# Performance work log

Measured on AMD Instinct MI355X. Metric: run time of the kernel, lower is better.

Reference implementation:

```python
import jax, jax.numpy as jnp
import numpy as np

N, T = 512, 48
VOCAB, EMBED, HIDDEN, IMG_DIM = 32000, 1024, 1024, 4096


def setup_inputs() -> dict:
    key = jax.random.key(0)
    ks = jax.random.split(key, 12)
    s = 0.02
    return {
        "questions": jax.random.randint(ks[0], (N, T), 0, VOCAB, dtype=jnp.int32),
        "img_features": jax.random.normal(ks[1], (N, IMG_DIM), dtype=jnp.float32),
        "emb": jax.random.normal(ks[2], (VOCAB, EMBED), dtype=jnp.float32) * s,
        "W_img": jax.random.normal(ks[3], (HIDDEN, IMG_DIM), dtype=jnp.float32) * s,
        "b_img": jnp.zeros((HIDDEN,), dtype=jnp.float32),
        "W_ih": jax.random.normal(ks[4], (4 * HIDDEN, EMBED), dtype=jnp.float32) * s,
        "W_hh": jax.random.normal(ks[5], (4 * HIDDEN, HIDDEN), dtype=jnp.float32) * s,
        "b_ih": jnp.zeros((4 * HIDDEN,), dtype=jnp.float32),
        "b_hh": jnp.zeros((4 * HIDDEN,), dtype=jnp.float32),
        "W_out": jax.random.normal(ks[6], (VOCAB, HIDDEN), dtype=jnp.float32) * s,
        "b_out": jnp.zeros((VOCAB,), dtype=jnp.float32),
        "first_words": 1,
    }


def reference(questions, img_features, emb, W_img, b_img, W_ih, W_hh, b_ih, b_hh,
              W_out, b_out, first_words):
    H = W_hh.shape[1]
    n = questions.shape[0]
    emb_q = emb[questions].transpose(1, 0, 2)          # [T, N, E]
    emb_i = img_features @ W_img.T + b_img             # [N, H]
    if first_words:
        seq = jnp.concatenate([emb_i[None], emb_q], axis=0)   # [T+1, N, E]
    else:
        seq = jnp.concatenate([emb_q, emb_i[None]], axis=0)

    def cell(carry, x_t):
        h, c = carry
        gates = x_t @ W_ih.T + b_ih + h @ W_hh.T + b_hh   # [N, 4H]
        i, f, g, o = jnp.split(gates, 4, axis=-1)          # torch LSTMCell gate order
        i, f, o = jax.nn.sigmoid(i), jax.nn.sigmoid(f), jax.nn.sigmoid(o)
        g = jnp.tanh(g)
        c = f * c + i * g
        h = o * jnp.tanh(c)
        return (h, c), h

    h0 = jnp.zeros((n, H), dtype=seq.dtype)
    (_, _), hs = jax.lax.scan(cell, (h0, h0), seq)     # hs: [T+1, N, H]
    hidden_states = hs.transpose(1, 0, 2)              # [N, T+1, H]
    output = hidden_states[:, -1, :] @ W_out.T + b_out  # [N, vocab]
    return output, hidden_states
```

## Files before the change

### kernel.cpp

```cpp
#include <hip/hip_runtime.h>
#include <hip/hip_bf16.h>
#include <stdint.h>

typedef __bf16 bf16_t;
typedef __attribute__((ext_vector_type(8))) __bf16 bf16x8;
typedef __attribute__((ext_vector_type(4))) __bf16 bf16x4;
typedef __attribute__((ext_vector_type(4))) float f32x4;
#define LL long long

__device__ __forceinline__ void gl_lds16(const bf16_t* g, bf16_t* s) {
  __builtin_amdgcn_global_load_lds(
      (const __attribute__((address_space(1))) void*)g,
      (__attribute__((address_space(3))) void*)s, 16, 0, 0);
}

__device__ __forceinline__ float sigm(float x) {
  return 1.0f / (1.0f + __expf(-x));
}
__device__ __forceinline__ float tanh_s(float x) {
  float e = __expf(-2.0f * fabsf(x));
  float t = (1.0f - e) / (1.0f + e);
  return copysignf(t, x);
}

template<int BM, int OUTBF>
__global__ __launch_bounds__(256, 2)
void gemm_bt(const bf16_t* __restrict__ A, const bf16_t* __restrict__ B,
             const float* __restrict__ bias,
             bf16_t* __restrict__ Cb, float* __restrict__ Cf,
             int N, int K, const int* __restrict__ fw, LL off0, LL off1) {
  __shared__ bf16_t lds_a[BM * 32];
  __shared__ bf16_t lds_b[128 * 32];
  const int tid = threadIdx.x;
  const int w = tid >> 6, l = tid & 63;
  const LL m0 = (LL)blockIdx.x * BM;
  const LL n0 = (LL)blockIdx.y * 128;
  constexpr int MI = BM / 32;
  const int wm = w & 1, wn = w >> 1;
  f32x4 acc[MI][4] = {};

  const int srow = l >> 2;
  const int scol = (l & 3) * 8;

  for (int kt = 0; kt < K; kt += 32) {
    for (int c = w; c < BM / 16; c += 4)
      gl_lds16(A + (m0 + c * 16 + srow) * K + kt + scol, &lds_a[c * 512]);
#pragma unroll
    for (int j = 0; j < 2; ++j) {
      int c = w * 2 + j;
      gl_lds16(B + (n0 + c * 16 + srow) * K + kt + scol, &lds_b[c * 512]);
    }
    __syncthreads();
    const int fr = l & 15, fk = (l >> 4) * 8;
    bf16x8 af[MI], bfr[4];
#pragma unroll
    for (int i = 0; i < MI; ++i)
      af[i] = *(const bf16x8*)&lds_a[(wm * (BM / 2) + i * 16 + fr) * 32 + fk];
#pragma unroll
    for (int j = 0; j < 4; ++j)
      bfr[j] = *(const bf16x8*)&lds_b[(wn * 64 + j * 16 + fr) * 32 + fk];
#pragma unroll
    for (int i = 0; i < MI; ++i)
#pragma unroll
      for (int j = 0; j < 4; ++j)
        acc[i][j] = __builtin_amdgcn_mfma_f32_16x16x32_bf16(af[i], bfr[j],
                                                            acc[i][j], 0, 0, 0);
    __syncthreads();
  }

  const LL coff = (fw[0] ? off1 : off0);
  const int er = (l >> 4) * 4, ec = l & 15;
#pragma unroll
  for (int i = 0; i < MI; ++i) {
#pragma unroll
    for (int j = 0; j < 4; ++j) {
      LL mrow = m0 + wm * (BM / 2) + i * 16 + er;
      LL ncol = n0 + wn * 64 + j * 16 + ec;
      float bs = bias[ncol];
#pragma unroll
      for (int r = 0; r < 4; ++r) {
        float v = acc[i][j][r] + bs;
        if (OUTBF) Cb[coff + (mrow + r) * N + ncol] = (bf16_t)v;
        else       Cf[(mrow + r) * N + ncol] = v;
      }
    }
  }
}

__global__ __launch_bounds__(256, 2)
void lstm_step(const bf16_t* __restrict__ h_in, const bf16_t* __restrict__ Whh,
               const bf16_t* __restrict__ Gt, float* __restrict__ c,
               bf16_t* __restrict__ h_out, float* __restrict__ hid, int t) {
  __shared__ bf16_t lds_a[64 * 32];
  __shared__ bf16_t lds_b[128 * 32];
  __shared__ float lds_ex[64 * 128];
  const int tid = threadIdx.x;
  const int w = tid >> 6, l = tid & 63;
  const int m0 = blockIdx.x * 64;
  const int n0 = blockIdx.y * 128;
  const int wm = w & 1, wn = w >> 1;
  f32x4 acc[2][4] = {};
  const int srow = l >> 2, scol = (l & 3) * 8;

  for (int kt = 0; kt < 1024; kt += 32) {
    gl_lds16(h_in + (LL)(m0 + w * 16 + srow) * 1024 + kt + scol,
             &lds_a[w * 512]);
#pragma unroll
    for (int j = 0; j < 2; ++j) {
      int ch = w * 2 + j;
      gl_lds16(Whh + (LL)(n0 + ch * 16 + srow) * 1024 + kt + scol,
               &lds_b[ch * 512]);
    }
    __syncthreads();
    const int fr = l & 15, fk = (l >> 4) * 8;
    bf16x8 af[2], bfr[4];
#pragma unroll
    for (int i = 0; i < 2; ++i)
      af[i] = *(const bf16x8*)&lds_a[(wm * 32 + i * 16 + fr) * 32 + fk];
#pragma unroll
    for (int j = 0; j < 4; ++j)
      bfr[j] = *(const bf16x8*)&lds_b[(wn * 64 + j * 16 + fr) * 32 + fk];
#pragma unroll
    for (int i = 0; i < 2; ++i)
#pragma unroll
      for (int j = 0; j < 4; ++j)
        acc[i][j] = __builtin_amdgcn_mfma_f32_16x16x32_bf16(af[i], bfr[j],
                                                            acc[i][j], 0, 0, 0);
    __syncthreads();
  }

  const int er = (l >> 4) * 4, ec = l & 15;
#pragma unroll
  for (int i = 0; i < 2; ++i)
#pragma unroll
    for (int j = 0; j < 4; ++j)
#pragma unroll
      for (int r = 0; r < 4; ++r)
        lds_ex[(wm * 32 + i * 16 + er + r) * 128 + wn * 64 + j * 16 + ec] =
            acc[i][j][r];
  __syncthreads();

  for (int cidx = tid; cidx < 2048; cidx += 256) {
    int ml = cidx >> 5, jl = cidx & 31;
    int m = m0 + ml;
    int j = (n0 >> 2) + jl;
    float4 ge = *(const float4*)&lds_ex[ml * 128 + jl * 4];
    bf16x4 g4 = *(const bf16x4*)(Gt + (LL)m * 4096 + n0 + jl * 4);
    float gi = ge.x + (float)g4[0];
    float gf = ge.y + (float)g4[1];
    float gg = ge.z + (float)g4[2];
    float go = ge.w + (float)g4[3];
    float iv = sigm(gi), fv = sigm(gf), gv = tanh_s(gg), ov = sigm(go);
    LL cij = (LL)m * 1024 + j;
    float cn = fv * c[cij] + iv * gv;
    float hn = ov * tanh_s(cn);
    c[cij] = cn;
    h_out[cij] = (bf16_t)hn;
    hid[((LL)m * 49 + t) * 1024 + j] = hn;
  }
}

__global__ __launch_bounds__(256)
void cvt_f2b(const float* __restrict__ src, bf16_t* __restrict__ dst, LL n4) {
  LL i = (LL)blockIdx.x * blockDim.x + threadIdx.x;
  LL stride = (LL)gridDim.x * blockDim.x;
  for (; i < n4; i += stride) {
    float4 v = *(const float4*)(src + i * 4);
    bf16x4 o;
    o[0] = (bf16_t)v.x; o[1] = (bf16_t)v.y; o[2] = (bf16_t)v.z; o[3] = (bf16_t)v.w;
    *(bf16x4*)(dst + i * 4) = o;
  }
}

__global__ __launch_bounds__(256)
void permute_w(const float* __restrict__ W, bf16_t* __restrict__ Wp) {
  int p = blockIdx.x;
  int r = (p & 3) * 1024 + (p >> 2);
  float4 v = *(const float4*)(W + (LL)r * 1024 + threadIdx.x * 4);
  bf16x4 o;
  o[0] = (bf16_t)v.x; o[1] = (bf16_t)v.y; o[2] = (bf16_t)v.z; o[3] = (bf16_t)v.w;
  *(bf16x4*)(Wp + (LL)p * 1024 + threadIdx.x * 4) = o;
}

__global__ __launch_bounds__(256)
void bias_comb(const float* __restrict__ bih, const float* __restrict__ bhh,
               float* __restrict__ bp) {
  int p = blockIdx.x * blockDim.x + threadIdx.x;
  int r = (p & 3) * 1024 + (p >> 2);
  bp[p] = bih[r] + bhh[r];
}

__global__ __launch_bounds__(256)
void gather_emb(const int* __restrict__ q, const float* __restrict__ emb,
                bf16_t* __restrict__ Xb, const int* __restrict__ fw) {
  int b = blockIdx.x;
  int tq = b >> 9;
  int n = b & 511;
  int slot = fw[0] ? tq + 1 : tq;
  int row = q[n * 48 + tq];
  float4 v = *(const float4*)(emb + (LL)row * 1024 + threadIdx.x * 4);
  bf16x4 o;
  o[0] = (bf16_t)v.x; o[1] = (bf16_t)v.y; o[2] = (bf16_t)v.z; o[3] = (bf16_t)v.w;
  *(bf16x4*)(Xb + ((LL)slot * 512 + n) * 1024 + threadIdx.x * 4) = o;
}

extern "C" void kernel_launch(void* const* d_in, const int* in_sizes, int n_in,
                              void* d_out, int out_size, void* d_ws,
                              size_t ws_size, hipStream_t stream) {
  const int*   questions = (const int*)  d_in[0];
  const float* img       = (const float*)d_in[1];
  const float* emb       = (const float*)d_in[2];
  const float* W_img     = (const float*)d_in[3];
  const float* b_img     = (const float*)d_in[4];
  const float* W_ih      = (const float*)d_in[5];
  const float* W_hh      = (const float*)d_in[6];
  const float* b_ih      = (const float*)d_in[7];
  const float* b_hh      = (const float*)d_in[8];
  const float* W_out     = (const float*)d_in[9];
  const float* b_out     = (const float*)d_in[10];
  const int*   fw        = (const int*)  d_in[11];

  char* ws = (char*)d_ws;
  size_t off = 0;
  auto alloc = [&](size_t bytes) {
    char* p = ws + off;
    off += (bytes + 255) & ~(size_t)255;
    return p;
  };
  bf16_t* Xb    = (bf16_t*)alloc((size_t)49 * 512 * 1024 * 2);
  bf16_t* G     = (bf16_t*)alloc((size_t)49 * 512 * 4096 * 2);
  bf16_t* Wp_ih = (bf16_t*)alloc((size_t)4096 * 1024 * 2);
  bf16_t* Wp_hh = (bf16_t*)alloc((size_t)4096 * 1024 * 2);
  bf16_t* Woutb = (bf16_t*)alloc((size_t)32000 * 1024 * 2);
  bf16_t* Wimgb = (bf16_t*)alloc((size_t)1024 * 4096 * 2);
  bf16_t* imgb  = (bf16_t*)alloc((size_t)512 * 4096 * 2);
  float*  biasp = (float*) alloc((size_t)4096 * 4);
  bf16_t* h0    = (bf16_t*)alloc((size_t)512 * 1024 * 2);
  bf16_t* h1    = (bf16_t*)alloc((size_t)512 * 1024 * 2);
  float*  cbuf  = (float*) alloc((size_t)512 * 1024 * 4);

  float* out0 = (float*)d_out;
  float* hid  = out0 + (size_t)512 * 32000;

  hipMemsetAsync(h0, 0, (size_t)512 * 1024 * 2, stream);
  hipMemsetAsync(cbuf, 0, (size_t)512 * 1024 * 4, stream);

  cvt_f2b<<<dim3(2048), dim3(256), 0, stream>>>(W_out, Woutb, (LL)32000 * 1024 / 4);
  cvt_f2b<<<dim3(1024), dim3(256), 0, stream>>>(W_img, Wimgb, (LL)1024 * 4096 / 4);
  cvt_f2b<<<dim3(512),  dim3(256), 0, stream>>>(img,   imgb,  (LL)512 * 4096 / 4);
  permute_w<<<dim3(4096), dim3(256), 0, stream>>>(W_ih, Wp_ih);
  permute_w<<<dim3(4096), dim3(256), 0, stream>>>(W_hh, Wp_hh);
  bias_comb<<<dim3(16), dim3(256), 0, stream>>>(b_ih, b_hh, biasp);
  gather_emb<<<dim3(48 * 512), dim3(256), 0, stream>>>(questions, emb, Xb, fw);

  gemm_bt<64, 1><<<dim3(8, 8), dim3(256), 0, stream>>>(
      imgb, Wimgb, b_img, Xb, nullptr, 1024, 4096, fw,
      (LL)48 * 512 * 1024, (LL)0);

  gemm_bt<128, 1><<<dim3(196, 32), dim3(256), 0, stream>>>(
      Xb, Wp_ih, biasp, G, nullptr, 4096, 1024, fw, 0, 0);

  for (int t = 0; t < 49; ++t) {
    const bf16_t* hin = (t & 1) ? h1 : h0;
    bf16_t* hout = (t & 1) ? h0 : h1;
    lstm_step<<<dim3(8, 32), dim3(256), 0, stream>>>(
        hin, Wp_hh, G + (LL)t * 512 * 4096, cbuf, hout, hid, t);
  }

  gemm_bt<128, 0><<<dim3(4, 250), dim3(256), 0, stream>>>(
      h1, Woutb, b_out, nullptr, out0, 32000, 1024, fw, 0, 0);
}
```

Measured before the change: 1.920 ms.

## Double-buffer LSTM step GEMM, shrink tiles to 64x64, remap blocks for L2 locality

```diff
diff --git a/kernel.cpp b/kernel.cpp
--- a/kernel.cpp
+++ b/kernel.cpp
@@ -91,41 +91,51 @@
 void lstm_step(const bf16_t* __restrict__ h_in, const bf16_t* __restrict__ Whh,
                const bf16_t* __restrict__ Gt, float* __restrict__ c,
                bf16_t* __restrict__ h_out, float* __restrict__ hid, int t) {
-  __shared__ bf16_t lds_a[64 * 32];
-  __shared__ bf16_t lds_b[128 * 32];
-  __shared__ float lds_ex[64 * 128];
+  __shared__ bf16_t lds_a[2][64 * 32];
+  __shared__ bf16_t lds_b[2][64 * 32];
+  __shared__ float lds_ex[64 * 64];
   const int tid = threadIdx.x;
   const int w = tid >> 6, l = tid & 63;
-  const int m0 = blockIdx.x * 64;
-  const int n0 = blockIdx.y * 128;
+  const int bid = blockIdx.x + (blockIdx.y << 3);
+  const int g = bid & 7, q = bid >> 3;
+  const int m0 = (q & 7) * 64;
+  const int n0 = ((g << 3) | (q >> 3)) * 64;
   const int wm = w & 1, wn = w >> 1;
-  f32x4 acc[2][4] = {};
+  f32x4 acc[2][2] = {};
   const int srow = l >> 2, scol = (l & 3) * 8;
-
-  for (int kt = 0; kt < 1024; kt += 32) {
+  const int fr = l & 15, fk = (l >> 4) * 8;
+
+  auto stage = [&](int buf, int kt) {
     gl_lds16(h_in + (LL)(m0 + w * 16 + srow) * 1024 + kt + scol,
-             &lds_a[w * 512]);
-#pragma unroll
-    for (int j = 0; j < 2; ++j) {
-      int ch = w * 2 + j;
-      gl_lds16(Whh + (LL)(n0 + ch * 16 + srow) * 1024 + kt + scol,
-               &lds_b[ch * 512]);
-    }
-    __syncthreads();
-    const int fr = l & 15, fk = (l >> 4) * 8;
-    bf16x8 af[2], bfr[4];
+             &lds_a[buf][w * 512]);
+    gl_lds16(Whh + (LL)(n0 + w * 16 + srow) * 1024 + kt + scol,
+             &lds_b[buf][w * 512]);
+  };
+  auto compute = [&](int buf) {
+    bf16x8 af[2], bfr[2];
 #pragma unroll
     for (int i = 0; i < 2; ++i)
-      af[i] = *(const bf16x8*)&lds_a[(wm * 32 + i * 16 + fr) * 32 + fk];
-#pragma unroll
-    for (int j = 0; j < 4; ++j)
-      bfr[j] = *(const bf16x8*)&lds_b[(wn * 64 + j * 16 + fr) * 32 + fk];
+      af[i] = *(const bf16x8*)&lds_a[buf][(wm * 32 + i * 16 + fr) * 32 + fk];
+#pragma unroll
+    for (int j = 0; j < 2; ++j)
+      bfr[j] = *(const bf16x8*)&lds_b[buf][(wn * 32 + j * 16 + fr) * 32 + fk];
 #pragma unroll
     for (int i = 0; i < 2; ++i)
 #pragma unroll
-      for (int j = 0; j < 4; ++j)
+      for (int j = 0; j < 2; ++j)
         acc[i][j] = __builtin_amdgcn_mfma_f32_16x16x32_bf16(af[i], bfr[j],
                                                             acc[i][j], 0, 0, 0);
+  };
+
+  stage(0, 0);
+  __syncthreads();
+#pragma unroll 1
+  for (int kt = 0; kt < 1024; kt += 64) {
+    stage(1, kt + 32);
+    compute(0);
+    __syncthreads();
+    if (kt + 64 < 1024) stage(0, kt + 64);
+    compute(1);
     __syncthreads();
   }
 
@@ -133,18 +143,18 @@
 #pragma unroll
   for (int i = 0; i < 2; ++i)
 #pragma unroll
-    for (int j = 0; j < 4; ++j)
+    for (int j = 0; j < 2; ++j)
 #pragma unroll
       for (int r = 0; r < 4; ++r)
-        lds_ex[(wm * 32 + i * 16 + er + r) * 128 + wn * 64 + j * 16 + ec] =
+        lds_ex[(wm * 32 + i * 16 + er + r) * 64 + wn * 32 + j * 16 + ec] =
             acc[i][j][r];
   __syncthreads();
 
-  for (int cidx = tid; cidx < 2048; cidx += 256) {
-    int ml = cidx >> 5, jl = cidx & 31;
+  for (int cidx = tid; cidx < 1024; cidx += 256) {
+    int ml = cidx >> 4, jl = cidx & 15;
     int m = m0 + ml;
     int j = (n0 >> 2) + jl;
-    float4 ge = *(const float4*)&lds_ex[ml * 128 + jl * 4];
+    float4 ge = *(const float4*)&lds_ex[ml * 64 + jl * 4];
     bf16x4 g4 = *(const bf16x4*)(Gt + (LL)m * 4096 + n0 + jl * 4);
     float gi = ge.x + (float)g4[0];
     float gf = ge.y + (float)g4[1];
@@ -263,7 +273,7 @@
   for (int t = 0; t < 49; ++t) {
     const bf16_t* hin = (t & 1) ? h1 : h0;
     bf16_t* hout = (t & 1) ? h0 : h1;
-    lstm_step<<<dim3(8, 32), dim3(256), 0, stream>>>(
+    lstm_step<<<dim3(8, 64), dim3(256), 0, stream>>>(
         hin, Wp_hh, G + (LL)t * 512 * 4096, cbuf, hout, hid, t);
   }
 
```

Result: faster. 1.604 ms (-16.4%).
